# Kernel optimization log

Measured on AMD Instinct MI355X. Metric: run time of the kernel, lower is better.

## Reference

```python
import jax, jax.numpy as jnp
import numpy as np
import math

TAU = 0.07
KD_T = 3.0
MOM = 0.5
POS_K = 1
NEG_K = 8192


def _kldiv(y_s, y_t, T):
    # F.kl_div(log_softmax(y_s/T), softmax(y_t/T), 'batchmean') * T^2
    log_ps = jax.nn.log_softmax(y_s / T, axis=1)
    log_pt = jax.nn.log_softmax(y_t / T, axis=1)
    pt = jnp.exp(log_pt)
    return jnp.sum(pt * (log_pt - log_ps)) / y_s.shape[0] * (T * T)


def setup_inputs() -> dict:
    key = jax.random.key(0)
    ks = jax.random.split(key, 6)
    B, D, N = 128, 128, 100000
    stdv = 1.0 / math.sqrt(D / 3)
    emb0 = jax.random.normal(ks[0], (B, D), dtype=jnp.float32)
    emb0 = emb0 / jnp.linalg.norm(emb0, axis=1, keepdims=True)
    emb1 = jax.random.normal(ks[1], (B, D), dtype=jnp.float32)
    emb1 = emb1 / jnp.linalg.norm(emb1, axis=1, keepdims=True)
    mem0 = jax.random.uniform(ks[2], (N, D), minval=-stdv, maxval=stdv, dtype=jnp.float32)
    mem1 = jax.random.uniform(ks[3], (N, D), minval=-stdv, maxval=stdv, dtype=jnp.float32)
    pos_idx = jax.random.randint(ks[4], (B, POS_K + 1), 0, N)
    neg_idx = jax.random.randint(ks[5], (B, NEG_K), 0, N)
    return {"emb0": emb0, "emb1": emb1, "mem0": mem0, "mem1": mem1,
            "pos_idx": pos_idx, "neg_idx": neg_idx}


def _simi(mem, emb, idx):
    # gather [B,K,D] rows from memory bank (detached) and dot with emb [B,D]
    rep = jax.lax.stop_gradient(mem[idx])
    return jnp.einsum('bkd,bd->bk', rep, emb) / TAU


def reference(emb0, emb1, mem0, mem1, pos_idx, neg_idx):
    embs = [emb0, emb1]
    mems = [mem0, mem1]
    n_net = 2
    idx = jnp.concatenate([pos_idx, neg_idx], axis=1)  # [B, 1+pos_k+neg_k]

    # ---- inter (cross-network) logits + soft ICL loss ----
    inter_logits = []
    soft_icl = jnp.float32(0.0)
    for i in range(n_net):
        for j in range(i + 1, n_net):
            cij = _simi(mems[i], embs[j], idx)
            cji = _simi(mems[j], embs[i], idx)
            inter_logits += [cij, cji]
            soft_icl = soft_icl + _kldiv(cij, jax.lax.stop_gradient(cji), KD_T)
            soft_icl = soft_icl + _kldiv(cji, jax.lax.stop_gradient(cij), KD_T)

    npos = POS_K + 1
    icl = jnp.float32(0.0)
    for logit in inter_logits:
        lp = logit - jax.nn.logsumexp(logit, axis=1, keepdims=True)
        icl = icl + (-jnp.mean(jnp.sum(lp[:, :npos], axis=1) / npos))

    # ---- intra (within-network) logits ----
    idx2 = idx[:, 1:]  # drop the first positive
    intra_logits = [_simi(mems[i], embs[i], idx2) for i in range(n_net)]

    soft_vcl = jnp.float32(0.0)
    for i in range(n_net):
        for j in range(n_net):
            if i != j:
                soft_vcl = soft_vcl + _kldiv(intra_logits[i], jax.lax.stop_gradient(intra_logits[j]), KD_T)

    vcl = jnp.float32(0.0)
    for logit in intra_logits:
        lp = logit - jax.nn.logsumexp(logit, axis=1, keepdims=True)
        vcl = vcl + (-jnp.mean(jnp.sum(lp[:, :POS_K], axis=1) / POS_K))

    # ---- momentum update + L2 normalize + scatter back (no grad) ----
    p0 = pos_idx[:, 0]
    new_mems = []
    for i in range(n_net):
        pos = mems[i][p0]
        upd = MOM * pos + (1.0 - MOM) * embs[i]
        upd = upd / jnp.sqrt(jnp.sum(upd * upd, axis=1, keepdims=True))
        new_mems.append(jax.lax.stop_gradient(mems[i].at[p0].set(upd)))

    return (vcl, soft_vcl, icl, soft_icl, new_mems[0], new_mems[1])
```

## Files before the change

kernel.cpp:

```cpp
#include <hip/hip_runtime.h>
#include <math.h>

#define B 128
#define D 128
#define NMEM 100000
#define KTOT 8194
#define NEGK 8192
#define CHUNKS 16
#define CS 513

__device__ __forceinline__ float half_allreduce(float v) {
    #pragma unroll
    for (int off = 1; off < 32; off <<= 1) v += __shfl_xor(v, off, 64);
    return v;
}

__global__ __launch_bounds__(256) void gather_logits(
        const float* __restrict__ emb0, const float* __restrict__ emb1,
        const float* __restrict__ mem0, const float* __restrict__ mem1,
        const int* __restrict__ pos_idx, const int* __restrict__ neg_idx,
        float* __restrict__ partials) {
    const int c = blockIdx.x;
    const int b = blockIdx.y;
    const int tid = threadIdx.x;
    const int lane = tid & 63;
    const int w = tid >> 6;
    const int half = lane >> 5;
    const int lane5 = lane & 31;
    const float INV_TAU = 1.0f / 0.07f;
    const float INV3 = 1.0f / 3.0f;

    const float4 q0 = *(const float4*)(emb0 + b * D + lane5 * 4);
    const float4 q1 = *(const float4*)(emb1 + b * D + lane5 * 4);

    float s1ij = 0.f, s1ji = 0.f, s1i0 = 0.f, s1i1 = 0.f;
    float s3ij = 0.f, s3ji = 0.f, s3i0 = 0.f, s3i1 = 0.f;
    float wa = 0.f, wb = 0.f, wc = 0.f, wd = 0.f;
    float sp0 = 0.f, sp1 = 0.f, sp2 = 0.f, sp3 = 0.f, sp4 = 0.f, sp5 = 0.f;

    const int k0 = c * CS;
    const int kend = (k0 + CS < KTOT) ? k0 + CS : KTOT;
    for (int kb = k0 + w * 2; kb < kend; kb += 8) {
        const int k = kb + half;
        const bool act = (k < kend);
        const int kc = act ? k : (kend - 1);
        const int r = (kc < 2) ? pos_idx[b * 2 + kc] : neg_idx[b * NEGK + (kc - 2)];
        const float4 m0 = *(const float4*)(mem0 + r * D + lane5 * 4);
        const float4 m1 = *(const float4*)(mem1 + r * D + lane5 * 4);
        float pij = m0.x * q1.x + m0.y * q1.y + m0.z * q1.z + m0.w * q1.w;
        float pii = m0.x * q0.x + m0.y * q0.y + m0.z * q0.z + m0.w * q0.w;
        float pji = m1.x * q0.x + m1.y * q0.y + m1.z * q0.z + m1.w * q0.w;
        float pjj = m1.x * q1.x + m1.y * q1.y + m1.z * q1.z + m1.w * q1.w;
        pij = half_allreduce(pij);
        pii = half_allreduce(pii);
        pji = half_allreduce(pji);
        pjj = half_allreduce(pjj);
        if (act) {
            const float cij = pij * INV_TAU, ci0 = pii * INV_TAU;
            const float cji = pji * INV_TAU, ci1 = pjj * INV_TAU;
            const float e3ij = __expf(cij * INV3), e3ji = __expf(cji * INV3);
            s1ij += __expf(cij);
            s1ji += __expf(cji);
            s3ij += e3ij;
            s3ji += e3ji;
            wa += e3ji * (cji - cij);
            wb += e3ij * (cij - cji);
            if (k >= 1) {
                const float e3i0 = __expf(ci0 * INV3), e3i1 = __expf(ci1 * INV3);
                s1i0 += __expf(ci0);
                s1i1 += __expf(ci1);
                s3i0 += e3i0;
                s3i1 += e3i1;
                wc += e3i1 * (ci1 - ci0);
                wd += e3i0 * (ci0 - ci1);
            }
            if (kc == 0) { sp0 = cij; sp2 = cji; }
            if (kc == 1) { sp1 = cij; sp3 = cji; sp4 = ci0; sp5 = ci1; }
        }
    }

    float v[12] = {s1ij, s1ji, s1i0, s1i1, s3ij, s3ji, s3i0, s3i1, wa, wb, wc, wd};
    #pragma unroll
    for (int j = 0; j < 12; ++j) v[j] += __shfl_xor(v[j], 32, 64);

    __shared__ float red[4][12];
    __shared__ float sps[6];
    if (lane == 0) {
        #pragma unroll
        for (int j = 0; j < 12; ++j) red[w][j] = v[j];
    }
    if (w == 0 && lane == 0) { sps[0] = sp0; sps[2] = sp2; }
    if (w == 0 && lane == 32) { sps[1] = sp1; sps[3] = sp3; sps[4] = sp4; sps[5] = sp5; }
    __syncthreads();
    float* outp = partials + (b * CHUNKS + c) * 20;
    if (tid < 12) outp[tid] = red[0][tid] + red[1][tid] + red[2][tid] + red[3][tid];
    else if (tid < 18) outp[tid] = sps[tid - 12];
}

__global__ void finalize(const float* __restrict__ partials, float* __restrict__ out) {
    const int b = threadIdx.x;
    float a[12];
    #pragma unroll
    for (int j = 0; j < 12; ++j) a[j] = 0.f;
    for (int c = 0; c < CHUNKS; ++c) {
        const float* p = partials + (b * CHUNKS + c) * 20;
        #pragma unroll
        for (int j = 0; j < 12; ++j) a[j] += p[j];
    }
    const float* e = partials + (b * CHUNKS) * 20 + 12;
    const float cij0 = e[0], cij1 = e[1], cji0 = e[2], cji1 = e[3], i01 = e[4], i11 = e[5];
    const float icl_b = -((cij0 + cij1) * 0.5f - __logf(a[0]))
                        - ((cji0 + cji1) * 0.5f - __logf(a[1]));
    const float vcl_b = -(i01 - __logf(a[2])) - (i11 - __logf(a[3]));
    const float sicl_b = 3.0f * (a[8] / a[5] + a[9] / a[4]);
    const float svcl_b = 3.0f * (a[10] / a[7] + a[11] / a[6]);
    __shared__ float r[4][128];
    r[0][b] = vcl_b; r[1][b] = svcl_b; r[2][b] = icl_b; r[3][b] = sicl_b;
    __syncthreads();
    for (int s = 64; s > 0; s >>= 1) {
        if (b < s) {
            r[0][b] += r[0][b + s]; r[1][b] += r[1][b + s];
            r[2][b] += r[2][b + s]; r[3][b] += r[3][b + s];
        }
        __syncthreads();
    }
    if (b == 0) {
        out[0] = r[0][0] * (1.0f / 128.f);
        out[1] = r[1][0] * (1.0f / 128.f);
        out[2] = r[2][0] * (1.0f / 128.f);
        out[3] = r[3][0] * (1.0f / 128.f);
    }
}

__global__ void copy_mems(const float4* __restrict__ m0, const float4* __restrict__ m1,
                          float4* __restrict__ o0, float4* __restrict__ o1) {
    const int n4 = NMEM * D / 4;
    for (int i = blockIdx.x * blockDim.x + threadIdx.x; i < n4; i += gridDim.x * blockDim.x) {
        o0[i] = m0[i];
        o1[i] = m1[i];
    }
}

__global__ void update_rows(const float* __restrict__ emb0, const float* __restrict__ emb1,
                            const float* __restrict__ mem0, const float* __restrict__ mem1,
                            const int* __restrict__ pos_idx,
                            float* __restrict__ o0, float* __restrict__ o1) {
    const int b = blockIdx.x;
    const int tid = threadIdx.x;
    const int lane = tid & 63;
    const int net = tid >> 6;
    const int p0 = pos_idx[b * 2];
    bool skip = false;
    for (int b2 = b + 1; b2 < B; ++b2)
        if (pos_idx[b2 * 2] == p0) skip = true;
    if (skip) return;
    const float* mem = net ? mem1 : mem0;
    const float* emb = net ? emb1 : emb0;
    float* o = net ? o1 : o0;
    const float2 mv = *(const float2*)(mem + p0 * D + 2 * lane);
    const float2 ev = *(const float2*)(emb + b * D + 2 * lane);
    const float ux = 0.5f * mv.x + 0.5f * ev.x;
    const float uy = 0.5f * mv.y + 0.5f * ev.y;
    float ss = ux * ux + uy * uy;
    #pragma unroll
    for (int off = 1; off < 64; off <<= 1) ss += __shfl_xor(ss, off, 64);
    const float inv = 1.0f / sqrtf(ss);
    float2 wv; wv.x = ux * inv; wv.y = uy * inv;
    *(float2*)(o + p0 * D + 2 * lane) = wv;
}

extern "C" void kernel_launch(void* const* d_in, const int* in_sizes, int n_in,
                              void* d_out, int out_size, void* d_ws, size_t ws_size,
                              hipStream_t stream) {
    const float* emb0 = (const float*)d_in[0];
    const float* emb1 = (const float*)d_in[1];
    const float* mem0 = (const float*)d_in[2];
    const float* mem1 = (const float*)d_in[3];
    const int* pos_idx = (const int*)d_in[4];
    const int* neg_idx = (const int*)d_in[5];
    float* out = (float*)d_out;
    float* partials = (float*)d_ws;

    float* out_m0 = out + 4;
    float* out_m1 = out + 4 + NMEM * D;

    gather_logits<<<dim3(CHUNKS, B), 256, 0, stream>>>(emb0, emb1, mem0, mem1,
                                                       pos_idx, neg_idx, partials);
    finalize<<<1, 128, 0, stream>>>(partials, out);
    copy_mems<<<4096, 256, 0, stream>>>((const float4*)mem0, (const float4*)mem1,
                                        (float4*)out_m0, (float4*)out_m1);
    update_rows<<<B, 128, 0, stream>>>(emb0, emb1, mem0, mem1, pos_idx, out_m0, out_m1);
}
```

Baseline: 376.9 us.

## Use eight-lane row groups with double-buffered gathers in logits kernel

Changes the gather kernel so each memory-bank row is handled by 8 lanes instead of 32. Each lane holds four float4 pieces of the row, and a wave processes 8 rows at once, which cuts the shuffle reduction to 3 steps. The row loads are software-pipelined with two register buffers, so the next row's gather is issued before the current row is computed. Branchy accumulation is replaced by multiplying by a 0/1 mask, and an occupancy hint is added to launch bounds. The cost is higher register pressure from the buffers and some exp work wasted on masked rows.

```diff
diff --git a/kernel.cpp b/kernel.cpp
--- a/kernel.cpp
+++ b/kernel.cpp
@@ -9,13 +9,7 @@
 #define CHUNKS 16
 #define CS 513
 
-__device__ __forceinline__ float half_allreduce(float v) {
-    #pragma unroll
-    for (int off = 1; off < 32; off <<= 1) v += __shfl_xor(v, off, 64);
-    return v;
-}
-
-__global__ __launch_bounds__(256) void gather_logits(
+__global__ __launch_bounds__(256, 4) void gather_logits(
         const float* __restrict__ emb0, const float* __restrict__ emb1,
         const float* __restrict__ mem0, const float* __restrict__ mem1,
         const int* __restrict__ pos_idx, const int* __restrict__ neg_idx,
@@ -25,72 +19,115 @@
     const int tid = threadIdx.x;
     const int lane = tid & 63;
     const int w = tid >> 6;
-    const int half = lane >> 5;
-    const int lane5 = lane & 31;
+    const int g = lane >> 3;
+    const int l8 = lane & 7;
     const float INV_TAU = 1.0f / 0.07f;
     const float INV3 = 1.0f / 3.0f;
 
-    const float4 q0 = *(const float4*)(emb0 + b * D + lane5 * 4);
-    const float4 q1 = *(const float4*)(emb1 + b * D + lane5 * 4);
+    float4 q0[4], q1[4];
+    #pragma unroll
+    for (int j = 0; j < 4; ++j) {
+        q0[j] = *(const float4*)(emb0 + b * D + j * 32 + l8 * 4);
+        q1[j] = *(const float4*)(emb1 + b * D + j * 32 + l8 * 4);
+    }
 
     float s1ij = 0.f, s1ji = 0.f, s1i0 = 0.f, s1i1 = 0.f;
     float s3ij = 0.f, s3ji = 0.f, s3i0 = 0.f, s3i1 = 0.f;
     float wa = 0.f, wb = 0.f, wc = 0.f, wd = 0.f;
-    float sp0 = 0.f, sp1 = 0.f, sp2 = 0.f, sp3 = 0.f, sp4 = 0.f, sp5 = 0.f;
+
+    __shared__ float red[4][12];
+    __shared__ float sps[6];
 
     const int k0 = c * CS;
     const int kend = (k0 + CS < KTOT) ? k0 + CS : KTOT;
-    for (int kb = k0 + w * 2; kb < kend; kb += 8) {
-        const int k = kb + half;
-        const bool act = (k < kend);
-        const int kc = act ? k : (kend - 1);
-        const int r = (kc < 2) ? pos_idx[b * 2 + kc] : neg_idx[b * NEGK + (kc - 2)];
-        const float4 m0 = *(const float4*)(mem0 + r * D + lane5 * 4);
-        const float4 m1 = *(const float4*)(mem1 + r * D + lane5 * 4);
-        float pij = m0.x * q1.x + m0.y * q1.y + m0.z * q1.z + m0.w * q1.w;
-        float pii = m0.x * q0.x + m0.y * q0.y + m0.z * q0.z + m0.w * q0.w;
-        float pji = m1.x * q0.x + m1.y * q0.y + m1.z * q0.z + m1.w * q0.w;
-        float pjj = m1.x * q1.x + m1.y * q1.y + m1.z * q1.z + m1.w * q1.w;
-        pij = half_allreduce(pij);
-        pii = half_allreduce(pii);
-        pji = half_allreduce(pji);
-        pjj = half_allreduce(pjj);
-        if (act) {
-            const float cij = pij * INV_TAU, ci0 = pii * INV_TAU;
-            const float cji = pji * INV_TAU, ci1 = pjj * INV_TAU;
-            const float e3ij = __expf(cij * INV3), e3ji = __expf(cji * INV3);
-            s1ij += __expf(cij);
-            s1ji += __expf(cji);
-            s3ij += e3ij;
-            s3ji += e3ji;
-            wa += e3ji * (cji - cij);
-            wb += e3ij * (cij - cji);
-            if (k >= 1) {
-                const float e3i0 = __expf(ci0 * INV3), e3i1 = __expf(ci1 * INV3);
-                s1i0 += __expf(ci0);
-                s1i1 += __expf(ci1);
-                s3i0 += e3i0;
-                s3i1 += e3i1;
-                wc += e3i1 * (ci1 - ci0);
-                wd += e3i0 * (ci0 - ci1);
-            }
-            if (kc == 0) { sp0 = cij; sp2 = cji; }
-            if (kc == 1) { sp1 = cij; sp3 = cji; sp4 = ci0; sp5 = ci1; }
-        }
-    }
+    const int kbase = k0 + w * 8 + g;
+    const int posbase = b * 2;
+    const int negbase = b * NEGK - 2;
+
+    if (tid < 6) sps[tid] = 0.f;
+
+    float4 A0[4], A1[4], B0[4], B1[4];
+
+#define FETCH(IT, R0, R1) do {                                               \
+    const int kf = kbase + (IT) * 32;                                        \
+    const int kc = (kf < kend) ? kf : (kend - 1);                            \
+    const int r = (kc < 2) ? pos_idx[posbase + kc] : neg_idx[negbase + kc];  \
+    const float* p0 = mem0 + r * D + l8 * 4;                                 \
+    const float* p1 = mem1 + r * D + l8 * 4;                                 \
+    _Pragma("unroll")                                                        \
+    for (int j = 0; j < 4; ++j) {                                            \
+        R0[j] = *(const float4*)(p0 + j * 32);                               \
+        R1[j] = *(const float4*)(p1 + j * 32);                               \
+    }                                                                        \
+} while (0)
+
+#define COMPUTE(IT, R0, R1) do {                                             \
+    const int kk = kbase + (IT) * 32;                                        \
+    float pij = 0.f, pii = 0.f, pji = 0.f, pjj = 0.f;                        \
+    _Pragma("unroll")                                                        \
+    for (int j = 0; j < 4; ++j) {                                            \
+        pij += R0[j].x * q1[j].x + R0[j].y * q1[j].y                         \
+             + R0[j].z * q1[j].z + R0[j].w * q1[j].w;                        \
+        pii += R0[j].x * q0[j].x + R0[j].y * q0[j].y                         \
+             + R0[j].z * q0[j].z + R0[j].w * q0[j].w;                        \
+        pji += R1[j].x * q0[j].x + R1[j].y * q0[j].y                         \
+             + R1[j].z * q0[j].z + R1[j].w * q0[j].w;                        \
+        pjj += R1[j].x * q1[j].x + R1[j].y * q1[j].y                         \
+             + R1[j].z * q1[j].z + R1[j].w * q1[j].w;                        \
+    }                                                                        \
+    _Pragma("unroll")                                                        \
+    for (int off = 1; off < 8; off <<= 1) {                                  \
+        pij += __shfl_xor(pij, off, 64);                                     \
+        pii += __shfl_xor(pii, off, 64);                                     \
+        pji += __shfl_xor(pji, off, 64);                                     \
+        pjj += __shfl_xor(pjj, off, 64);                                     \
+    }                                                                        \
+    const float mA = (kk < kend) ? 1.f : 0.f;                                \
+    const float mI = (kk >= 1) ? mA : 0.f;                                   \
+    const float cij = pij * INV_TAU, ci0 = pii * INV_TAU;                    \
+    const float cji = pji * INV_TAU, ci1 = pjj * INV_TAU;                    \
+    const float e3ij = __expf(cij * INV3), e3ji = __expf(cji * INV3);        \
+    const float e3i0 = __expf(ci0 * INV3), e3i1 = __expf(ci1 * INV3);        \
+    s1ij += mA * __expf(cij);                                                \
+    s1ji += mA * __expf(cji);                                                \
+    s3ij += mA * e3ij;                                                       \
+    s3ji += mA * e3ji;                                                       \
+    wa += mA * e3ji * (cji - cij);                                           \
+    wb += mA * e3ij * (cij - cji);                                           \
+    s1i0 += mI * __expf(ci0);                                                \
+    s1i1 += mI * __expf(ci1);                                                \
+    s3i0 += mI * e3i0;                                                       \
+    s3i1 += mI * e3i1;                                                       \
+    wc += mI * e3i1 * (ci1 - ci0);                                           \
+    wd += mI * e3i0 * (ci0 - ci1);                                           \
+    if (kk == 0 && l8 == 0) { sps[0] = cij; sps[2] = cji; }                  \
+    if (kk == 1 && l8 == 0) { sps[1] = cij; sps[3] = cji;                    \
+                              sps[4] = ci0; sps[5] = ci1; }                  \
+} while (0)
+
+    FETCH(0, A0, A1);
+    for (int it = 0; it < 16; it += 2) {
+        FETCH(it + 1, B0, B1);
+        COMPUTE(it, A0, A1);
+        FETCH(it + 2, A0, A1);
+        COMPUTE(it + 1, B0, B1);
+    }
+    COMPUTE(16, A0, A1);
+
+#undef FETCH
+#undef COMPUTE
 
     float v[12] = {s1ij, s1ji, s1i0, s1i1, s3ij, s3ji, s3i0, s3i1, wa, wb, wc, wd};
     #pragma unroll
-    for (int j = 0; j < 12; ++j) v[j] += __shfl_xor(v[j], 32, 64);
-
-    __shared__ float red[4][12];
-    __shared__ float sps[6];
+    for (int j = 0; j < 12; ++j) {
+        v[j] += __shfl_xor(v[j], 8, 64);
+        v[j] += __shfl_xor(v[j], 16, 64);
+        v[j] += __shfl_xor(v[j], 32, 64);
+    }
     if (lane == 0) {
         #pragma unroll
         for (int j = 0; j < 12; ++j) red[w][j] = v[j];
     }
-    if (w == 0 && lane == 0) { sps[0] = sp0; sps[2] = sp2; }
-    if (w == 0 && lane == 32) { sps[1] = sp1; sps[3] = sp3; sps[4] = sp4; sps[5] = sp5; }
     __syncthreads();
     float* outp = partials + (b * CHUNKS + c) * 20;
     if (tid < 12) outp[tid] = red[0][tid] + red[1][tid] + red[2][tid] + red[3][tid];
```

Result: faster. 339.6 us (-9.9%).
